# Kernel tuning notes

Measured on AMD Instinct MI355X. Metric: run time of the kernel, lower is better.

The kernel has to match this reference:

```python
import jax, jax.numpy as jnp
import numpy as np

N_NODES = 100000
N_EDGES = 3200000
IN_DIM, HID_DIM, LAT_DIM = 128, 64, 64


def gcn_conv(x, edge_index, W, b):
    """PyG-style GCNConv: add self-loops, symmetric deg^-1/2 normalization,
    linear transform, scatter-add aggregation, bias."""
    N = x.shape[0]
    loops = jnp.arange(N, dtype=edge_index.dtype)
    src = jnp.concatenate([edge_index[0], loops])  # [E+N]
    dst = jnp.concatenate([edge_index[1], loops])  # [E+N]
    # degree on target index (with self loops)
    deg = jax.ops.segment_sum(jnp.ones_like(dst, dtype=x.dtype), dst, num_segments=N)
    dinv = jnp.where(deg > 0, jax.lax.rsqrt(deg), 0.0)
    norm = dinv[src] * dinv[dst]  # [E+N]
    h = x @ W  # [N, out_dim] -- transform BEFORE gather (out_dim <= in_dim)
    msg = h[src] * norm[:, None]  # [E+N, out_dim]
    out = jax.ops.segment_sum(msg, dst, num_segments=N)
    return out + b


def setup_inputs() -> dict:
    key = jax.random.key(0)
    ks = jax.random.split(key, 6)
    x = jax.random.normal(ks[0], (N_NODES, IN_DIM), dtype=jnp.float32)
    edge_index = jax.random.randint(ks[1], (2, N_EDGES), 0, N_NODES, dtype=jnp.int64)
    # Glorot-ish init for weights, zero bias (PyG default)
    W1 = jax.random.normal(ks[2], (IN_DIM, HID_DIM), dtype=jnp.float32) / np.sqrt(IN_DIM)
    b1 = jnp.zeros((HID_DIM,), dtype=jnp.float32)
    W2 = jax.random.normal(ks[3], (HID_DIM, LAT_DIM), dtype=jnp.float32) / np.sqrt(HID_DIM)
    b2 = jnp.zeros((LAT_DIM,), dtype=jnp.float32)
    return {"x": x, "edge_index": edge_index, "W1": W1, "b1": b1, "W2": W2, "b2": b2}


def reference(x, edge_index, W1, b1, W2, b2):
    h = jax.nn.relu(gcn_conv(x, edge_index, W1, b1))
    return gcn_conv(h, edge_index, W2, b2)
```

## Files before the change

### kernel.cpp

```cpp
#include <hip/hip_runtime.h>
#include <cstdint>


#define BSHIFT 7
#define NBMAX 784
#define CH 8192
#define MAXB 6016

typedef __attribute__((ext_vector_type(8))) short bf16x8;
typedef __attribute__((ext_vector_type(4))) float f32x4;

__device__ inline unsigned short f2bf(float f) {
    unsigned u = __float_as_uint(f);
    unsigned r = (u + 0x7FFFu + ((u >> 16) & 1u)) >> 16;
    return (unsigned short)r;
}
__device__ inline unsigned pack2(float a, float b) {
    return (unsigned)f2bf(a) | ((unsigned)f2bf(b) << 16);
}
__device__ inline float blo(unsigned u) { return __uint_as_float(u << 16); }
__device__ inline float bhi(unsigned u) { return __uint_as_float(u & 0xFFFF0000u); }

__global__ __launch_bounds__(256) void hist_kernel(const int* __restrict__ dst,
                                                   int* __restrict__ histmat,
                                                   int E, int nb, int nblk,
                                                   const float* __restrict__ W1,
                                                   const float* __restrict__ W2,
                                                   unsigned short* __restrict__ W1t,
                                                   unsigned short* __restrict__ W2t) {
    if (blockIdx.x >= (unsigned)nblk) {
        int i = (blockIdx.x - nblk) * 256 + threadIdx.x;
        if (i < 128 * 64) {
            int k = i >> 6, n = i & 63;
            W1t[n * 128 + k] = f2bf(W1[i]);
        }
        int j = i - 128 * 64;
        if (j >= 0 && j < 64 * 64) {
            int k = j >> 6, n = j & 63;
            W2t[n * 64 + k] = f2bf(W2[j]);
        }
        return;
    }
    __shared__ int hist[NBMAX];
    int t = threadIdx.x;
    for (int b = t; b < nb; b += 256) hist[b] = 0;
    __syncthreads();
    int base = blockIdx.x * CH;
#pragma unroll
    for (int j = 0; j < CH / 1024; ++j) {
        int idx = base + j * 1024 + t * 4;
        if (idx + 4 <= E) {
            int4 d = *(const int4*)(dst + idx);
            atomicAdd(&hist[d.x >> BSHIFT], 1);
            atomicAdd(&hist[d.y >> BSHIFT], 1);
            atomicAdd(&hist[d.z >> BSHIFT], 1);
            atomicAdd(&hist[d.w >> BSHIFT], 1);
        } else {
            for (int k = 0; k < 4; ++k)
                if (idx + k < E) atomicAdd(&hist[dst[idx + k] >> BSHIFT], 1);
        }
    }
    __syncthreads();
    for (int b = t; b < nb; b += 256) histmat[blockIdx.x * nb + b] = hist[b];
}

__global__ __launch_bounds__(256) void scancol_kernel(const int* __restrict__ histmat,
                                                      int* __restrict__ colbase,
                                                      int* __restrict__ buckettotal,
                                                      int nb, int nblk) {
    __shared__ int ts[256];
    int b = blockIdx.x;
    int t = threadIdx.x;
    int v[4];
    int tsum = 0;
#pragma unroll
    for (int k = 0; k < 4; ++k) {
        int blk = t * 4 + k;
        v[k] = (blk < nblk) ? histmat[blk * nb + b] : 0;
        tsum += v[k];
    }
    ts[t] = tsum;
    __syncthreads();
    for (int ofs = 1; ofs < 256; ofs <<= 1) {
        int val = (t >= ofs) ? ts[t - ofs] : 0;
        __syncthreads();
        ts[t] += val;
        __syncthreads();
    }
    int run = ts[t] - tsum;
#pragma unroll
    for (int k = 0; k < 4; ++k) {
        int blk = t * 4 + k;
        if (blk < nblk) colbase[blk * nb + b] = run;
        run += v[k];
    }
    if (t == 255) buckettotal[b] = ts[255];
}

__global__ __launch_bounds__(256) void bscatter_kernel(const int* __restrict__ src,
                                                       const int* __restrict__ dst,
                                                       const int* __restrict__ colbase,
                                                       const int* __restrict__ buckettotal,
                                                       int* __restrict__ packed,
                                                       int E, int nb) {
    __shared__ int cur[NBMAX];
    __shared__ int ts2[256];
    int t = threadIdx.x;
    int v4[4];
    int tsum = 0;
#pragma unroll
    for (int k = 0; k < 4; ++k) {
        int bb = t * 4 + k;
        v4[k] = (bb < nb) ? buckettotal[bb] : 0;
        tsum += v4[k];
    }
    ts2[t] = tsum;
    __syncthreads();
    for (int ofs = 1; ofs < 256; ofs <<= 1) {
        int val = (t >= ofs) ? ts2[t - ofs] : 0;
        __syncthreads();
        ts2[t] += val;
        __syncthreads();
    }
    int run = ts2[t] - tsum;
#pragma unroll
    for (int k = 0; k < 4; ++k) {
        int bb = t * 4 + k;
        if (bb < nb) cur[bb] = run + colbase[blockIdx.x * nb + bb];
        run += v4[k];
    }
    __syncthreads();
    int base = blockIdx.x * CH;
#pragma unroll
    for (int j = 0; j < CH / 1024; ++j) {
        int idx = base + j * 1024 + t * 4;
        if (idx + 4 <= E) {
            int4 d = *(const int4*)(dst + idx);
            int4 s = *(const int4*)(src + idx);
            int p;
            p = atomicAdd(&cur[d.x >> BSHIFT], 1); packed[p] = ((d.x & 127) << 17) | s.x;
            p = atomicAdd(&cur[d.y >> BSHIFT], 1); packed[p] = ((d.y & 127) << 17) | s.y;
            p = atomicAdd(&cur[d.z >> BSHIFT], 1); packed[p] = ((d.z & 127) << 17) | s.z;
            p = atomicAdd(&cur[d.w >> BSHIFT], 1); packed[p] = ((d.w & 127) << 17) | s.w;
        } else {
            for (int k = 0; k < 4; ++k)
                if (idx + k < E) {
                    int dd = dst[idx + k], ss = src[idx + k];
                    int p = atomicAdd(&cur[dd >> BSHIFT], 1);
                    packed[p] = ((dd & 127) << 17) | ss;
                }
        }
    }
}

__global__ __launch_bounds__(256) void bcsr_kernel(const int* __restrict__ packed,
                                                   const int* __restrict__ buckettotal,
                                                   int* __restrict__ rowptr,
                                                   float* __restrict__ dinv,
                                                   int* __restrict__ csr,
                                                   int N, int nb) {
    __shared__ int deg[128];
    __shared__ int lrp[128];
    __shared__ int ts[128];
    __shared__ int ts2[256];
    __shared__ int shbb[2];
    __shared__ int ebuf[MAXB];
    __shared__ int obuf[MAXB];
    int b = blockIdx.x;
    int t = threadIdx.x;
    if (t < 128) deg[t] = 0;
    int v4[4];
    int tsum = 0;
#pragma unroll
    for (int k = 0; k < 4; ++k) {
        int bb = t * 4 + k;
        v4[k] = (bb < nb) ? buckettotal[bb] : 0;
        tsum += v4[k];
    }
    ts2[t] = tsum;
    __syncthreads();
    for (int ofs = 1; ofs < 256; ofs <<= 1) {
        int val = (t >= ofs) ? ts2[t - ofs] : 0;
        __syncthreads();
        ts2[t] += val;
        __syncthreads();
    }
    int run = ts2[t] - tsum;
#pragma unroll
    for (int k = 0; k < 4; ++k) {
        int bb = t * 4 + k;
        if (bb == b) { shbb[0] = run; shbb[1] = run + v4[k]; }
        run += v4[k];
    }
    __syncthreads();
    int bb0 = shbb[0];
    int bb1 = shbb[1];
    int cnt = bb1 - bb0;
    bool fits = (cnt <= MAXB);
    if (fits) {
        for (int i = t; i < cnt; i += 256) {
            int v = packed[bb0 + i];
            ebuf[i] = v;
            atomicAdd(&deg[v >> 17], 1);
        }
    } else {
        for (int i = t; i < cnt; i += 256)
            atomicAdd(&deg[packed[bb0 + i] >> 17], 1);
    }
    __syncthreads();
    if (t < 128) ts[t] = deg[t];
    __syncthreads();
    for (int ofs = 1; ofs < 128; ofs <<= 1) {
        int v = (t < 128 && t >= ofs) ? ts[t - ofs] : 0;
        __syncthreads();
        if (t < 128) ts[t] += v;
        __syncthreads();
    }
    int node0 = b << BSHIFT;
    int nlocal = min(128, N - node0);
    if (t < 128) lrp[t] = ts[t] - deg[t];
    if (t < nlocal) {
        rowptr[node0 + t] = bb0 + (ts[t] - deg[t]);
        dinv[node0 + t] = rsqrtf((float)(deg[t] + 1));
    }
    if (t == nlocal) rowptr[node0 + nlocal] = bb1;
    __syncthreads();
    if (fits) {
        for (int i = t; i < cnt; i += 256) {
            int v = ebuf[i];
            int p = atomicAdd(&lrp[v >> 17], 1);
            obuf[p] = v & 0x1FFFF;
        }
        __syncthreads();
        for (int i = t; i < cnt; i += 256) csr[bb0 + i] = obuf[i];
    } else {
        for (int i = t; i < cnt; i += 256) {
            int v = packed[bb0 + i];
            int p = atomicAdd(&lrp[v >> 17], 1);
            csr[bb0 + p] = v & 0x1FFFF;
        }
    }
}

template <int K, bool XBF16>
__global__ __launch_bounds__(256) void gemm_mfma(const void* __restrict__ Xv,
                                                 const unsigned short* __restrict__ Wt,
                                                 const float* __restrict__ dinv,
                                                 unsigned short* __restrict__ Ybf, int M) {
    constexpr int KP = K + 8;
    __shared__ unsigned short Xs[64 * KP];
    __shared__ unsigned short Ws[64 * KP];
    int t = threadIdx.x;
    int row0 = blockIdx.x * 64;

    for (int i = t; i < 64 * K / 8; i += 256) {
        int r = i / (K / 8), c8 = i % (K / 8);
        *(uint4*)(&Ws[r * KP + c8 * 8]) = ((const uint4*)Wt)[i];
    }
    if (XBF16) {
        const unsigned short* X = (const unsigned short*)Xv;
        for (int i = t; i < 64 * K / 8; i += 256) {
            int r = i / (K / 8), c8 = i % (K / 8);
            int gr = row0 + r;
            uint4 v = make_uint4(0u, 0u, 0u, 0u);
            if (gr < M) v = ((const uint4*)(X + (size_t)gr * K))[c8];
            *(uint4*)(&Xs[r * KP + c8 * 8]) = v;
        }
    } else {
        const float* X = (const float*)Xv;
        for (int i = t; i < 64 * K / 4; i += 256) {
            int r = i / (K / 4), c4 = i % (K / 4);
            int gr = row0 + r;
            float4 v = make_float4(0.f, 0.f, 0.f, 0.f);
            if (gr < M) v = ((const float4*)(X + (size_t)gr * K))[c4];
            uint2 p;
            p.x = pack2(v.x, v.y);
            p.y = pack2(v.z, v.w);
            *(uint2*)(&Xs[r * KP + c4 * 4]) = p;
        }
    }
    __syncthreads();

    int lane = t & 63;
    int w = t >> 6;
    int m = lane & 15;
    int q = lane >> 4;

    f32x4 acc[4];
#pragma unroll
    for (int nt = 0; nt < 4; ++nt) acc[nt] = (f32x4){0.f, 0.f, 0.f, 0.f};

#pragma unroll
    for (int s = 0; s < K / 32; ++s) {
        bf16x8 a = *(const bf16x8*)(&Xs[(16 * w + m) * KP + s * 32 + q * 8]);
#pragma unroll
        for (int nt = 0; nt < 4; ++nt) {
            bf16x8 b = *(const bf16x8*)(&Ws[(16 * nt + m) * KP + s * 32 + q * 8]);
            acc[nt] = __builtin_amdgcn_mfma_f32_16x16x32_bf16(a, b, acc[nt], 0, 0, 0);
        }
    }
    __syncthreads();

    unsigned short* Cs = Xs;
#pragma unroll
    for (int nt = 0; nt < 4; ++nt)
#pragma unroll
        for (int r = 0; r < 4; ++r) {
            int row = 16 * w + q * 4 + r;
            int gr = row0 + row;
            float d = (gr < M) ? dinv[gr] : 0.f;
            Cs[row * 72 + nt * 16 + m] = f2bf(acc[nt][r] * d);
        }
    __syncthreads();
    for (int i = t; i < 64 * 64 / 8; i += 256) {
        int r = i >> 3, c8 = i & 7;
        int gr = row0 + r;
        if (gr < M)
            *(uint4*)(Ybf + (size_t)gr * 64 + c8 * 8) = *(const uint4*)(&Cs[r * 72 + c8 * 8]);
    }
}

#define ACC8(v)                                      \
    acc[0] += blo(v.x); acc[1] += bhi(v.x);          \
    acc[2] += blo(v.y); acc[3] += bhi(v.y);          \
    acc[4] += blo(v.z); acc[5] += bhi(v.z);          \
    acc[6] += blo(v.w); acc[7] += bhi(v.w);

template <bool DO_GEMM>
__global__ __launch_bounds__(256) void aggregate_kernel(const unsigned* __restrict__ hsu,
                                                        const int* __restrict__ rowptr,
                                                        const int* __restrict__ csr,
                                                        const float* __restrict__ dinv,
                                                        const float* __restrict__ bias,
                                                        const unsigned short* __restrict__ W2t,
                                                        void* __restrict__ outv, int N) {
    __shared__ unsigned short Hs[DO_GEMM ? 32 * 72 : 1];
    __shared__ unsigned short W2s[DO_GEMM ? 64 * 72 : 1];
    __shared__ unsigned short Cs[DO_GEMM ? 32 * 72 : 1];
    int t = threadIdx.x;
    int node0 = blockIdx.x * 32;
    int node = node0 + (t >> 3);
    int sub = t & 7;
    int gbase = t & 56;

    if (DO_GEMM) {
        for (int i = t; i < 64 * 64 / 8; i += 256) {
            int r = i >> 3, c8 = i & 7;
            *(uint4*)(&W2s[r * 72 + c8 * 8]) = ((const uint4*)W2t)[i];
        }
    }

    float acc[8] = {0.f, 0.f, 0.f, 0.f, 0.f, 0.f, 0.f, 0.f};
    if (node < N) {
        {
            uint4 v = *(const uint4*)(hsu + (size_t)node * 32 + sub * 4);
            acc[0] = blo(v.x); acc[1] = bhi(v.x);
            acc[2] = blo(v.y); acc[3] = bhi(v.y);
            acc[4] = blo(v.z); acc[5] = bhi(v.z);
            acc[6] = blo(v.w); acc[7] = bhi(v.w);
        }
        int e0 = rowptr[node];
        int e1 = rowptr[node + 1];
        int e = e0;
        for (; e + 8 <= e1; e += 8) {
            int idx = csr[e + sub];
            int s0 = __shfl(idx, gbase + 0, 64);
            int s1 = __shfl(idx, gbase + 1, 64);
            int s2 = __shfl(idx, gbase + 2, 64);
            int s3 = __shfl(idx, gbase + 3, 64);
            int s4 = __shfl(idx, gbase + 4, 64);
            int s5 = __shfl(idx, gbase + 5, 64);
            int s6 = __shfl(idx, gbase + 6, 64);
            int s7 = __shfl(idx, gbase + 7, 64);
            uint4 v0 = *(const uint4*)(hsu + (size_t)s0 * 32 + sub * 4);
            uint4 v1 = *(const uint4*)(hsu + (size_t)s1 * 32 + sub * 4);
            uint4 v2 = *(const uint4*)(hsu + (size_t)s2 * 32 + sub * 4);
            uint4 v3 = *(const uint4*)(hsu + (size_t)s3 * 32 + sub * 4);
            uint4 v4 = *(const uint4*)(hsu + (size_t)s4 * 32 + sub * 4);
            uint4 v5 = *(const uint4*)(hsu + (size_t)s5 * 32 + sub * 4);
            uint4 v6 = *(const uint4*)(hsu + (size_t)s6 * 32 + sub * 4);
            uint4 v7 = *(const uint4*)(hsu + (size_t)s7 * 32 + sub * 4);
            ACC8(v0); ACC8(v1); ACC8(v2); ACC8(v3);
            ACC8(v4); ACC8(v5); ACC8(v6); ACC8(v7);
        }
        for (; e < e1; ++e) {
            int s = csr[e];
            uint4 v = *(const uint4*)(hsu + (size_t)s * 32 + sub * 4);
            ACC8(v);
        }
    }

    if (DO_GEMM) {
        if (node < N) {
            float d = dinv[node];
            float4 b0 = *(const float4*)(bias + sub * 8);
            float4 b1 = *(const float4*)(bias + sub * 8 + 4);
            float o[8];
            o[0] = fmaxf(fmaf(acc[0], d, b0.x), 0.f);
            o[1] = fmaxf(fmaf(acc[1], d, b0.y), 0.f);
            o[2] = fmaxf(fmaf(acc[2], d, b0.z), 0.f);
            o[3] = fmaxf(fmaf(acc[3], d, b0.w), 0.f);
            o[4] = fmaxf(fmaf(acc[4], d, b1.x), 0.f);
            o[5] = fmaxf(fmaf(acc[5], d, b1.y), 0.f);
            o[6] = fmaxf(fmaf(acc[6], d, b1.z), 0.f);
            o[7] = fmaxf(fmaf(acc[7], d, b1.w), 0.f);
            uint4 p;
            p.x = pack2(o[0], o[1]); p.y = pack2(o[2], o[3]);
            p.z = pack2(o[4], o[5]); p.w = pack2(o[6], o[7]);
            *(uint4*)(&Hs[(t >> 3) * 72 + sub * 8]) = p;
        }
        __syncthreads();
        int lane = t & 63;
        int w = t >> 6;
        int m = lane & 15;
        int q = lane >> 4;
        int mt = w & 1;
#pragma unroll
        for (int half = 0; half < 2; ++half) {
            int nt = (w >> 1) + half * 2;
            f32x4 a4 = (f32x4){0.f, 0.f, 0.f, 0.f};
#pragma unroll
            for (int s = 0; s < 2; ++s) {
                bf16x8 a = *(const bf16x8*)(&Hs[(mt * 16 + m) * 72 + s * 32 + q * 8]);
                bf16x8 b = *(const bf16x8*)(&W2s[(nt * 16 + m) * 72 + s * 32 + q * 8]);
                a4 = __builtin_amdgcn_mfma_f32_16x16x32_bf16(a, b, a4, 0, 0, 0);
            }
#pragma unroll
            for (int r = 0; r < 4; ++r) {
                int row = mt * 16 + q * 4 + r;
                int gn = node0 + row;
                float dd = (gn < N) ? dinv[gn] : 0.f;
                Cs[row * 72 + nt * 16 + m] = f2bf(a4[r] * dd);
            }
        }
        __syncthreads();
        unsigned short* outb = (unsigned short*)outv;
        for (int i = t; i < 32 * 64 / 8; i += 256) {
            int r = i >> 3, c8 = i & 7;
            int gn = node0 + r;
            if (gn < N)
                *(uint4*)(outb + (size_t)gn * 64 + c8 * 8) = *(const uint4*)(&Cs[r * 72 + c8 * 8]);
        }
    } else {
        if (node >= N) return;
        float d = dinv[node];
        float4 b0 = *(const float4*)(bias + sub * 8);
        float4 b1 = *(const float4*)(bias + sub * 8 + 4);
        float o[8];
        o[0] = fmaf(acc[0], d, b0.x); o[1] = fmaf(acc[1], d, b0.y);
        o[2] = fmaf(acc[2], d, b0.z); o[3] = fmaf(acc[3], d, b0.w);
        o[4] = fmaf(acc[4], d, b1.x); o[5] = fmaf(acc[5], d, b1.y);
        o[6] = fmaf(acc[6], d, b1.z); o[7] = fmaf(acc[7], d, b1.w);
        float* op = (float*)outv + (size_t)node * 64 + sub * 8;
        *(float4*)(op)     = make_float4(o[0], o[1], o[2], o[3]);
        *(float4*)(op + 4) = make_float4(o[4], o[5], o[6], o[7]);
    }
}

extern "C" void kernel_launch(void* const* d_in, const int* in_sizes, int n_in,
                              void* d_out, int out_size, void* d_ws, size_t ws_size,
                              hipStream_t stream) {
    const float* x  = (const float*)d_in[0];
    const int*   ei = (const int*)d_in[1];
    const float* W1 = (const float*)d_in[2];
    const float* b1 = (const float*)d_in[3];
    const float* W2 = (const float*)d_in[4];
    const float* b2 = (const float*)d_in[5];

    const int N = in_sizes[0] / 128;
    const int E = in_sizes[1] / 2;
    const int* src = ei;
    const int* dst = ei + E;
    float* out = (float*)d_out;

    const int nb   = (N + 127) >> BSHIFT;
    const int nblk = (E + CH - 1) / CH;

    char* ws = (char*)d_ws;
    size_t off = 0;
    auto alloc = [&](size_t bytes) -> char* {
        char* p = ws + off;
        off = (off + bytes + 255) & ~(size_t)255;
        return p;
    };
    int*   csr         = (int*)alloc((size_t)E * 4);
    int*   rowptr      = (int*)alloc((size_t)(N + 1) * 4);
    float* dinv        = (float*)alloc((size_t)N * 4);
    int*   buckettotal = (int*)alloc((size_t)nb * 4);
    unsigned short* W1t = (unsigned short*)alloc(64 * 128 * 2);
    unsigned short* W2t = (unsigned short*)alloc(64 * 64 * 2);
    unsigned short* bufA = (unsigned short*)alloc((size_t)N * 64 * 2);
    unsigned short* bufB = (unsigned short*)alloc((size_t)N * 64 * 2);
    int* histmat = (int*)bufA;
    int* packed  = (int*)((char*)bufA + ((size_t)nblk * nb * 4 + 255 & ~(size_t)255) + 256);

    hist_kernel<<<nblk + 48, 256, 0, stream>>>(dst, histmat, E, nb, nblk, W1, W2, W1t, W2t);
    scancol_kernel<<<nb, 256, 0, stream>>>(histmat, histmat, buckettotal, nb, nblk);
    bscatter_kernel<<<nblk, 256, 0, stream>>>(src, dst, histmat, buckettotal, packed, E, nb);
    bcsr_kernel<<<nb, 256, 0, stream>>>(packed, buckettotal, rowptr, dinv, csr, N, nb);

    gemm_mfma<128, false><<<(N + 63) / 64, 256, 0, stream>>>(x, W1t, dinv, bufA, N);
    aggregate_kernel<true><<<(N + 31) / 32, 256, 0, stream>>>((const unsigned*)bufA, rowptr,
                                                              csr, dinv, b1, W2t, bufB, N);
    aggregate_kernel<false><<<(N + 31) / 32, 256, 0, stream>>>((const unsigned*)bufB, rowptr,
                                                               csr, dinv, b2, W2t, out, N);
}
```

Baseline: 310.2 us.

## Compute degrees in histogram pass and fuse bucket scatter with first GEMM

Per-node degrees are now counted with global atomics during the histogram pass, so dinv can be written early in the column-scan kernel. That lets the first GEMM run in the same launch as the bucket scatter. The scatter blocks now handle larger chunks of edges, and bcsr no longer counts degrees itself. The layer-1 aggregate now does its W2 matmul per wave, with register shuffles instead of a block-wide shared tile. The cost is 3.2M extra global atomics, an extra memset, and reuse of the csr and bufB buffers as scratch.

```diff
diff --git a/kernel.cpp b/kernel.cpp
--- a/kernel.cpp
+++ b/kernel.cpp
@@ -4,11 +4,14 @@
 
 #define BSHIFT 7
 #define NBMAX 784
-#define CH 8192
+#define CHH 8192
+#define CHC 32768
 #define MAXB 6016
 
 typedef __attribute__((ext_vector_type(8))) short bf16x8;
 typedef __attribute__((ext_vector_type(4))) float f32x4;
+
+union U8 { unsigned u[4]; bf16x8 v; };
 
 __device__ inline unsigned short f2bf(float f) {
     unsigned u = __float_as_uint(f);
@@ -27,7 +30,8 @@
                                                    const float* __restrict__ W1,
                                                    const float* __restrict__ W2,
                                                    unsigned short* __restrict__ W1t,
-                                                   unsigned short* __restrict__ W2t) {
+                                                   unsigned short* __restrict__ W2t,
+                                                   int* __restrict__ deg_g) {
     if (blockIdx.x >= (unsigned)nblk) {
         int i = (blockIdx.x - nblk) * 256 + threadIdx.x;
         if (i < 128 * 64) {
@@ -45,9 +49,9 @@
     int t = threadIdx.x;
     for (int b = t; b < nb; b += 256) hist[b] = 0;
     __syncthreads();
-    int base = blockIdx.x * CH;
-#pragma unroll
-    for (int j = 0; j < CH / 1024; ++j) {
+    int base = blockIdx.x * CHH;
+#pragma unroll
+    for (int j = 0; j < CHH / 1024; ++j) {
         int idx = base + j * 1024 + t * 4;
         if (idx + 4 <= E) {
             int4 d = *(const int4*)(dst + idx);
@@ -55,9 +59,17 @@
             atomicAdd(&hist[d.y >> BSHIFT], 1);
             atomicAdd(&hist[d.z >> BSHIFT], 1);
             atomicAdd(&hist[d.w >> BSHIFT], 1);
+            atomicAdd(&deg_g[d.x], 1);
+            atomicAdd(&deg_g[d.y], 1);
+            atomicAdd(&deg_g[d.z], 1);
+            atomicAdd(&deg_g[d.w], 1);
         } else {
             for (int k = 0; k < 4; ++k)
-                if (idx + k < E) atomicAdd(&hist[dst[idx + k] >> BSHIFT], 1);
+                if (idx + k < E) {
+                    int dd = dst[idx + k];
+                    atomicAdd(&hist[dd >> BSHIFT], 1);
+                    atomicAdd(&deg_g[dd], 1);
+                }
         }
     }
     __syncthreads();
@@ -67,10 +79,16 @@
 __global__ __launch_bounds__(256) void scancol_kernel(const int* __restrict__ histmat,
                                                       int* __restrict__ colbase,
                                                       int* __restrict__ buckettotal,
-                                                      int nb, int nblk) {
+                                                      int nb, int nblk,
+                                                      const int* __restrict__ deg_g,
+                                                      float* __restrict__ dinv, int N) {
     __shared__ int ts[256];
     int b = blockIdx.x;
     int t = threadIdx.x;
+    if (t < 128) {
+        int node = b * 128 + t;
+        if (node < N) dinv[node] = rsqrtf((float)(deg_g[node] + 1));
+    }
     int v[4];
     int tsum = 0;
 #pragma unroll
@@ -97,15 +115,86 @@
     if (t == 255) buckettotal[b] = ts[255];
 }
 
-__global__ __launch_bounds__(256) void bscatter_kernel(const int* __restrict__ src,
-                                                       const int* __restrict__ dst,
-                                                       const int* __restrict__ colbase,
-                                                       const int* __restrict__ buckettotal,
-                                                       int* __restrict__ packed,
-                                                       int E, int nb) {
-    __shared__ int cur[NBMAX];
-    __shared__ int ts2[256];
-    int t = threadIdx.x;
+__device__ void gemm1_body(char* smem, const float* __restrict__ X,
+                           const unsigned short* __restrict__ Wt,
+                           const float* __restrict__ dinv,
+                           unsigned short* __restrict__ Ybf, int M, int blk) {
+    constexpr int K = 128, KP = 136;
+    unsigned short* Xs = (unsigned short*)smem;
+    unsigned short* Ws = Xs + 64 * KP;
+    int t = threadIdx.x;
+    int row0 = blk * 64;
+
+    for (int i = t; i < 64 * K / 8; i += 256) {
+        int r = i / (K / 8), c8 = i % (K / 8);
+        *(uint4*)(&Ws[r * KP + c8 * 8]) = ((const uint4*)Wt)[i];
+    }
+    for (int i = t; i < 64 * K / 4; i += 256) {
+        int r = i / (K / 4), c4 = i % (K / 4);
+        int gr = row0 + r;
+        float4 v = make_float4(0.f, 0.f, 0.f, 0.f);
+        if (gr < M) v = ((const float4*)(X + (size_t)gr * K))[c4];
+        uint2 p;
+        p.x = pack2(v.x, v.y);
+        p.y = pack2(v.z, v.w);
+        *(uint2*)(&Xs[r * KP + c4 * 4]) = p;
+    }
+    __syncthreads();
+
+    int lane = t & 63;
+    int w = t >> 6;
+    int m = lane & 15;
+    int q = lane >> 4;
+
+    f32x4 acc[4];
+#pragma unroll
+    for (int nt = 0; nt < 4; ++nt) acc[nt] = (f32x4){0.f, 0.f, 0.f, 0.f};
+
+#pragma unroll
+    for (int s = 0; s < K / 32; ++s) {
+        bf16x8 a = *(const bf16x8*)(&Xs[(16 * w + m) * KP + s * 32 + q * 8]);
+#pragma unroll
+        for (int nt = 0; nt < 4; ++nt) {
+            bf16x8 b = *(const bf16x8*)(&Ws[(16 * nt + m) * KP + s * 32 + q * 8]);
+            acc[nt] = __builtin_amdgcn_mfma_f32_16x16x32_bf16(a, b, acc[nt], 0, 0, 0);
+        }
+    }
+    __syncthreads();
+
+    unsigned short* Cs = Xs;
+#pragma unroll
+    for (int nt = 0; nt < 4; ++nt)
+#pragma unroll
+        for (int r = 0; r < 4; ++r) {
+            int row = 16 * w + q * 4 + r;
+            int gr = row0 + row;
+            float d = (gr < M) ? dinv[gr] : 0.f;
+            Cs[row * 72 + nt * 16 + m] = f2bf(acc[nt][r] * d);
+        }
+    __syncthreads();
+    for (int i = t; i < 64 * 64 / 8; i += 256) {
+        int r = i >> 3, c8 = i & 7;
+        int gr = row0 + r;
+        if (gr < M)
+            *(uint4*)(Ybf + (size_t)gr * 64 + c8 * 8) = *(const uint4*)(&Cs[r * 72 + c8 * 8]);
+    }
+}
+
+__global__ __launch_bounds__(256) void bscatter_gemm1_kernel(
+        const int* __restrict__ src, const int* __restrict__ dst,
+        const int* __restrict__ colbase, const int* __restrict__ buckettotal,
+        int* __restrict__ packed, int E, int nb, int nblkc,
+        const float* __restrict__ x, const unsigned short* __restrict__ W1t,
+        const float* __restrict__ dinv, unsigned short* __restrict__ bufA, int N) {
+    __shared__ char smem[2 * 64 * 136 * 2];
+    int t = threadIdx.x;
+    if ((int)blockIdx.x >= nblkc) {
+        gemm1_body(smem, x, W1t, dinv, bufA, N, (int)blockIdx.x - nblkc);
+        return;
+    }
+    int* cur = (int*)smem;
+    int* ts2 = cur + NBMAX;
+    int c0 = (int)blockIdx.x * (CHC / CHH);
     int v4[4];
     int tsum = 0;
 #pragma unroll
@@ -126,13 +215,13 @@
 #pragma unroll
     for (int k = 0; k < 4; ++k) {
         int bb = t * 4 + k;
-        if (bb < nb) cur[bb] = run + colbase[blockIdx.x * nb + bb];
+        if (bb < nb) cur[bb] = run + colbase[(size_t)c0 * nb + bb];
         run += v4[k];
     }
     __syncthreads();
-    int base = blockIdx.x * CH;
-#pragma unroll
-    for (int j = 0; j < CH / 1024; ++j) {
+    int base = (int)blockIdx.x * CHC;
+#pragma unroll 4
+    for (int j = 0; j < CHC / 1024; ++j) {
         int idx = base + j * 1024 + t * 4;
         if (idx + 4 <= E) {
             int4 d = *(const int4*)(dst + idx);
@@ -142,7 +231,7 @@
             p = atomicAdd(&cur[d.y >> BSHIFT], 1); packed[p] = ((d.y & 127) << 17) | s.y;
             p = atomicAdd(&cur[d.z >> BSHIFT], 1); packed[p] = ((d.z & 127) << 17) | s.z;
             p = atomicAdd(&cur[d.w >> BSHIFT], 1); packed[p] = ((d.w & 127) << 17) | s.w;
-        } else {
+        } else if (idx < E) {
             for (int k = 0; k < 4; ++k)
                 if (idx + k < E) {
                     int dd = dst[idx + k], ss = src[idx + k];
@@ -155,8 +244,8 @@
 
 __global__ __launch_bounds__(256) void bcsr_kernel(const int* __restrict__ packed,
                                                    const int* __restrict__ buckettotal,
+                                                   const int* __restrict__ deg_g,
                                                    int* __restrict__ rowptr,
-                                                   float* __restrict__ dinv,
                                                    int* __restrict__ csr,
                                                    int N, int nb) {
     __shared__ int deg[128];
@@ -168,7 +257,11 @@
     __shared__ int obuf[MAXB];
     int b = blockIdx.x;
     int t = threadIdx.x;
-    if (t < 128) deg[t] = 0;
+    int node0 = b << BSHIFT;
+    if (t < 128) {
+        int node = node0 + t;
+        deg[t] = (node < N) ? deg_g[node] : 0;
+    }
     int v4[4];
     int tsum = 0;
 #pragma unroll
@@ -198,16 +291,8 @@
     int cnt = bb1 - bb0;
     bool fits = (cnt <= MAXB);
     if (fits) {
-        for (int i = t; i < cnt; i += 256) {
-            int v = packed[bb0 + i];
-            ebuf[i] = v;
-            atomicAdd(&deg[v >> 17], 1);
-        }
-    } else {
-        for (int i = t; i < cnt; i += 256)
-            atomicAdd(&deg[packed[bb0 + i] >> 17], 1);
-    }
-    __syncthreads();
+        for (int i = t; i < cnt; i += 256) ebuf[i] = packed[bb0 + i];
+    }
     if (t < 128) ts[t] = deg[t];
     __syncthreads();
     for (int ofs = 1; ofs < 128; ofs <<= 1) {
@@ -216,13 +301,9 @@
         if (t < 128) ts[t] += v;
         __syncthreads();
     }
-    int node0 = b << BSHIFT;
     int nlocal = min(128, N - node0);
     if (t < 128) lrp[t] = ts[t] - deg[t];
-    if (t < nlocal) {
-        rowptr[node0 + t] = bb0 + (ts[t] - deg[t]);
-        dinv[node0 + t] = rsqrtf((float)(deg[t] + 1));
-    }
+    if (t < nlocal) rowptr[node0 + t] = bb0 + (ts[t] - deg[t]);
     if (t == nlocal) rowptr[node0 + nlocal] = bb1;
     __syncthreads();
     if (fits) {
@@ -242,219 +323,160 @@
     }
 }
 
-template <int K, bool XBF16>
-__global__ __launch_bounds__(256) void gemm_mfma(const void* __restrict__ Xv,
-                                                 const unsigned short* __restrict__ Wt,
-                                                 const float* __restrict__ dinv,
-                                                 unsigned short* __restrict__ Ybf, int M) {
-    constexpr int KP = K + 8;
-    __shared__ unsigned short Xs[64 * KP];
-    __shared__ unsigned short Ws[64 * KP];
-    int t = threadIdx.x;
-    int row0 = blockIdx.x * 64;
-
-    for (int i = t; i < 64 * K / 8; i += 256) {
-        int r = i / (K / 8), c8 = i % (K / 8);
-        *(uint4*)(&Ws[r * KP + c8 * 8]) = ((const uint4*)Wt)[i];
-    }
-    if (XBF16) {
-        const unsigned short* X = (const unsigned short*)Xv;
-        for (int i = t; i < 64 * K / 8; i += 256) {
-            int r = i / (K / 8), c8 = i % (K / 8);
-            int gr = row0 + r;
-            uint4 v = make_uint4(0u, 0u, 0u, 0u);
-            if (gr < M) v = ((const uint4*)(X + (size_t)gr * K))[c8];
-            *(uint4*)(&Xs[r * KP + c8 * 8]) = v;
-        }
-    } else {
-        const float* X = (const float*)Xv;
-        for (int i = t; i < 64 * K / 4; i += 256) {
-            int r = i / (K / 4), c4 = i % (K / 4);
-            int gr = row0 + r;
-            float4 v = make_float4(0.f, 0.f, 0.f, 0.f);
-            if (gr < M) v = ((const float4*)(X + (size_t)gr * K))[c4];
-            uint2 p;
-            p.x = pack2(v.x, v.y);
-            p.y = pack2(v.z, v.w);
-            *(uint2*)(&Xs[r * KP + c4 * 4]) = p;
-        }
-    }
-    __syncthreads();
-
-    int lane = t & 63;
-    int w = t >> 6;
-    int m = lane & 15;
-    int q = lane >> 4;
-
-    f32x4 acc[4];
-#pragma unroll
-    for (int nt = 0; nt < 4; ++nt) acc[nt] = (f32x4){0.f, 0.f, 0.f, 0.f};
-
-#pragma unroll
-    for (int s = 0; s < K / 32; ++s) {
-        bf16x8 a = *(const bf16x8*)(&Xs[(16 * w + m) * KP + s * 32 + q * 8]);
-#pragma unroll
-        for (int nt = 0; nt < 4; ++nt) {
-            bf16x8 b = *(const bf16x8*)(&Ws[(16 * nt + m) * KP + s * 32 + q * 8]);
-            acc[nt] = __builtin_amdgcn_mfma_f32_16x16x32_bf16(a, b, acc[nt], 0, 0, 0);
-        }
-    }
-    __syncthreads();
-
-    unsigned short* Cs = Xs;
-#pragma unroll
-    for (int nt = 0; nt < 4; ++nt)
-#pragma unroll
-        for (int r = 0; r < 4; ++r) {
-            int row = 16 * w + q * 4 + r;
-            int gr = row0 + row;
-            float d = (gr < M) ? dinv[gr] : 0.f;
-            Cs[row * 72 + nt * 16 + m] = f2bf(acc[nt][r] * d);
-        }
-    __syncthreads();
-    for (int i = t; i < 64 * 64 / 8; i += 256) {
-        int r = i >> 3, c8 = i & 7;
-        int gr = row0 + r;
-        if (gr < M)
-            *(uint4*)(Ybf + (size_t)gr * 64 + c8 * 8) = *(const uint4*)(&Cs[r * 72 + c8 * 8]);
-    }
-}
-
 #define ACC8(v)                                      \
     acc[0] += blo(v.x); acc[1] += bhi(v.x);          \
     acc[2] += blo(v.y); acc[3] += bhi(v.y);          \
     acc[4] += blo(v.z); acc[5] += bhi(v.z);          \
     acc[6] += blo(v.w); acc[7] += bhi(v.w);
 
-template <bool DO_GEMM>
-__global__ __launch_bounds__(256) void aggregate_kernel(const unsigned* __restrict__ hsu,
-                                                        const int* __restrict__ rowptr,
-                                                        const int* __restrict__ csr,
-                                                        const float* __restrict__ dinv,
-                                                        const float* __restrict__ bias,
-                                                        const unsigned short* __restrict__ W2t,
-                                                        void* __restrict__ outv, int N) {
-    __shared__ unsigned short Hs[DO_GEMM ? 32 * 72 : 1];
-    __shared__ unsigned short W2s[DO_GEMM ? 64 * 72 : 1];
-    __shared__ unsigned short Cs[DO_GEMM ? 32 * 72 : 1];
-    int t = threadIdx.x;
+#define GATHER_BODY                                                     \
+    {                                                                   \
+        uint4 v = *(const uint4*)(hsu + (size_t)node * 32 + sub * 4);   \
+        acc[0] = blo(v.x); acc[1] = bhi(v.x);                           \
+        acc[2] = blo(v.y); acc[3] = bhi(v.y);                           \
+        acc[4] = blo(v.z); acc[5] = bhi(v.z);                           \
+        acc[6] = blo(v.w); acc[7] = bhi(v.w);                           \
+    }                                                                   \
+    int e0 = rowptr[node];                                              \
+    int e1 = rowptr[node + 1];                                          \
+    int e = e0;                                                         \
+    for (; e + 8 <= e1; e += 8) {                                       \
+        int idx = csr[e + sub];                                         \
+        int s0 = __shfl(idx, gbase + 0, 64);                            \
+        int s1 = __shfl(idx, gbase + 1, 64);                            \
+        int s2 = __shfl(idx, gbase + 2, 64);                            \
+        int s3 = __shfl(idx, gbase + 3, 64);                            \
+        int s4 = __shfl(idx, gbase + 4, 64);                            \
+        int s5 = __shfl(idx, gbase + 5, 64);                            \
+        int s6 = __shfl(idx, gbase + 6, 64);                            \
+        int s7 = __shfl(idx, gbase + 7, 64);                            \
+        uint4 v0 = *(const uint4*)(hsu + (size_t)s0 * 32 + sub * 4);    \
+        uint4 v1 = *(const uint4*)(hsu + (size_t)s1 * 32 + sub * 4);    \
+        uint4 v2 = *(const uint4*)(hsu + (size_t)s2 * 32 + sub * 4);    \
+        uint4 v3 = *(const uint4*)(hsu + (size_t)s3 * 32 + sub * 4);    \
+        uint4 v4 = *(const uint4*)(hsu + (size_t)s4 * 32 + sub * 4);    \
+        uint4 v5 = *(const uint4*)(hsu + (size_t)s5 * 32 + sub * 4);    \
+        uint4 v6 = *(const uint4*)(hsu + (size_t)s6 * 32 + sub * 4);    \
+        uint4 v7 = *(const uint4*)(hsu + (size_t)s7 * 32 + sub * 4);    \
+        ACC8(v0); ACC8(v1); ACC8(v2); ACC8(v3);                         \
+        ACC8(v4); ACC8(v5); ACC8(v6); ACC8(v7);                         \
+    }                                                                   \
+    for (; e < e1; ++e) {                                               \
+        int s = csr[e];                                                 \
+        uint4 v = *(const uint4*)(hsu + (size_t)s * 32 + sub * 4);      \
+        ACC8(v);                                                        \
+    }
+
+__global__ __launch_bounds__(256) void aggregate_gemm_kernel(
+        const unsigned* __restrict__ hsu, const int* __restrict__ rowptr,
+        const int* __restrict__ csr, const float* __restrict__ dinv,
+        const float* __restrict__ bias, const unsigned short* __restrict__ W2t,
+        unsigned short* __restrict__ outb, int N) {
+    __shared__ unsigned short W2s[64 * 72];
+    __shared__ unsigned short Cs[4][8 * 72];
+    int t = threadIdx.x;
+    for (int i = t; i < 64 * 64 / 8; i += 256) {
+        int r = i >> 3, c8 = i & 7;
+        *(uint4*)(&W2s[r * 72 + c8 * 8]) = ((const uint4*)W2t)[i];
+    }
+    __syncthreads();
+
     int node0 = blockIdx.x * 32;
     int node = node0 + (t >> 3);
     int sub = t & 7;
     int gbase = t & 56;
 
-    if (DO_GEMM) {
-        for (int i = t; i < 64 * 64 / 8; i += 256) {
-            int r = i >> 3, c8 = i & 7;
-            *(uint4*)(&W2s[r * 72 + c8 * 8]) = ((const uint4*)W2t)[i];
-        }
-    }
-
     float acc[8] = {0.f, 0.f, 0.f, 0.f, 0.f, 0.f, 0.f, 0.f};
+    uint4 pk = make_uint4(0u, 0u, 0u, 0u);
     if (node < N) {
-        {
-            uint4 v = *(const uint4*)(hsu + (size_t)node * 32 + sub * 4);
-            acc[0] = blo(v.x); acc[1] = bhi(v.x);
-            acc[2] = blo(v.y); acc[3] = bhi(v.y);
-            acc[4] = blo(v.z); acc[5] = bhi(v.z);
-            acc[6] = blo(v.w); acc[7] = bhi(v.w);
-        }
-        int e0 = rowptr[node];
-        int e1 = rowptr[node + 1];
-        int e = e0;
-        for (; e + 8 <= e1; e += 8) {
-            int idx = csr[e + sub];
-            int s0 = __shfl(idx, gbase + 0, 64);
-            int s1 = __shfl(idx, gbase + 1, 64);
-            int s2 = __shfl(idx, gbase + 2, 64);
-            int s3 = __shfl(idx, gbase + 3, 64);
-            int s4 = __shfl(idx, gbase + 4, 64);
-            int s5 = __shfl(idx, gbase + 5, 64);
-            int s6 = __shfl(idx, gbase + 6, 64);
-            int s7 = __shfl(idx, gbase + 7, 64);
-            uint4 v0 = *(const uint4*)(hsu + (size_t)s0 * 32 + sub * 4);
-            uint4 v1 = *(const uint4*)(hsu + (size_t)s1 * 32 + sub * 4);
-            uint4 v2 = *(const uint4*)(hsu + (size_t)s2 * 32 + sub * 4);
-            uint4 v3 = *(const uint4*)(hsu + (size_t)s3 * 32 + sub * 4);
-            uint4 v4 = *(const uint4*)(hsu + (size_t)s4 * 32 + sub * 4);
-            uint4 v5 = *(const uint4*)(hsu + (size_t)s5 * 32 + sub * 4);
-            uint4 v6 = *(const uint4*)(hsu + (size_t)s6 * 32 + sub * 4);
-            uint4 v7 = *(const uint4*)(hsu + (size_t)s7 * 32 + sub * 4);
-            ACC8(v0); ACC8(v1); ACC8(v2); ACC8(v3);
-            ACC8(v4); ACC8(v5); ACC8(v6); ACC8(v7);
-        }
-        for (; e < e1; ++e) {
-            int s = csr[e];
-            uint4 v = *(const uint4*)(hsu + (size_t)s * 32 + sub * 4);
-            ACC8(v);
-        }
-    }
-
-    if (DO_GEMM) {
-        if (node < N) {
-            float d = dinv[node];
-            float4 b0 = *(const float4*)(bias + sub * 8);
-            float4 b1 = *(const float4*)(bias + sub * 8 + 4);
-            float o[8];
-            o[0] = fmaxf(fmaf(acc[0], d, b0.x), 0.f);
-            o[1] = fmaxf(fmaf(acc[1], d, b0.y), 0.f);
-            o[2] = fmaxf(fmaf(acc[2], d, b0.z), 0.f);
-            o[3] = fmaxf(fmaf(acc[3], d, b0.w), 0.f);
-            o[4] = fmaxf(fmaf(acc[4], d, b1.x), 0.f);
-            o[5] = fmaxf(fmaf(acc[5], d, b1.y), 0.f);
-            o[6] = fmaxf(fmaf(acc[6], d, b1.z), 0.f);
-            o[7] = fmaxf(fmaf(acc[7], d, b1.w), 0.f);
-            uint4 p;
-            p.x = pack2(o[0], o[1]); p.y = pack2(o[2], o[3]);
-            p.z = pack2(o[4], o[5]); p.w = pack2(o[6], o[7]);
-            *(uint4*)(&Hs[(t >> 3) * 72 + sub * 8]) = p;
-        }
-        __syncthreads();
-        int lane = t & 63;
-        int w = t >> 6;
-        int m = lane & 15;
-        int q = lane >> 4;
-        int mt = w & 1;
-#pragma unroll
-        for (int half = 0; half < 2; ++half) {
-            int nt = (w >> 1) + half * 2;
-            f32x4 a4 = (f32x4){0.f, 0.f, 0.f, 0.f};
-#pragma unroll
-            for (int s = 0; s < 2; ++s) {
-                bf16x8 a = *(const bf16x8*)(&Hs[(mt * 16 + m) * 72 + s * 32 + q * 8]);
-                bf16x8 b = *(const bf16x8*)(&W2s[(nt * 16 + m) * 72 + s * 32 + q * 8]);
-                a4 = __builtin_amdgcn_mfma_f32_16x16x32_bf16(a, b, a4, 0, 0, 0);
-            }
-#pragma unroll
-            for (int r = 0; r < 4; ++r) {
-                int row = mt * 16 + q * 4 + r;
-                int gn = node0 + row;
-                float dd = (gn < N) ? dinv[gn] : 0.f;
-                Cs[row * 72 + nt * 16 + m] = f2bf(a4[r] * dd);
-            }
-        }
-        __syncthreads();
-        unsigned short* outb = (unsigned short*)outv;
-        for (int i = t; i < 32 * 64 / 8; i += 256) {
-            int r = i >> 3, c8 = i & 7;
-            int gn = node0 + r;
-            if (gn < N)
-                *(uint4*)(outb + (size_t)gn * 64 + c8 * 8) = *(const uint4*)(&Cs[r * 72 + c8 * 8]);
-        }
-    } else {
-        if (node >= N) return;
+        GATHER_BODY
         float d = dinv[node];
         float4 b0 = *(const float4*)(bias + sub * 8);
         float4 b1 = *(const float4*)(bias + sub * 8 + 4);
-        float o[8];
-        o[0] = fmaf(acc[0], d, b0.x); o[1] = fmaf(acc[1], d, b0.y);
-        o[2] = fmaf(acc[2], d, b0.z); o[3] = fmaf(acc[3], d, b0.w);
-        o[4] = fmaf(acc[4], d, b1.x); o[5] = fmaf(acc[5], d, b1.y);
-        o[6] = fmaf(acc[6], d, b1.z); o[7] = fmaf(acc[7], d, b1.w);
-        float* op = (float*)outv + (size_t)node * 64 + sub * 8;
-        *(float4*)(op)     = make_float4(o[0], o[1], o[2], o[3]);
-        *(float4*)(op + 4) = make_float4(o[4], o[5], o[6], o[7]);
-    }
+        float o0 = fmaxf(fmaf(acc[0], d, b0.x), 0.f);
+        float o1 = fmaxf(fmaf(acc[1], d, b0.y), 0.f);
+        float o2 = fmaxf(fmaf(acc[2], d, b0.z), 0.f);
+        float o3 = fmaxf(fmaf(acc[3], d, b0.w), 0.f);
+        float o4 = fmaxf(fmaf(acc[4], d, b1.x), 0.f);
+        float o5 = fmaxf(fmaf(acc[5], d, b1.y), 0.f);
+        float o6 = fmaxf(fmaf(acc[6], d, b1.z), 0.f);
+        float o7 = fmaxf(fmaf(acc[7], d, b1.w), 0.f);
+        pk.x = pack2(o0, o1); pk.y = pack2(o2, o3);
+        pk.z = pack2(o4, o5); pk.w = pack2(o6, o7);
+    }
+
+    int lane = t & 63;
+    int m16 = lane & 15;
+    int q = lane >> 4;
+    int wv = t >> 6;
+    int wnode0 = node0 + wv * 8;
+    bool am = (m16 < 8);
+    int sl0 = ((m16 & 7) << 3) + q;
+    int sl1 = sl0 + 4;
+    unsigned a00 = (unsigned)__shfl((int)pk.x, sl0, 64);
+    unsigned a01 = (unsigned)__shfl((int)pk.y, sl0, 64);
+    unsigned a02 = (unsigned)__shfl((int)pk.z, sl0, 64);
+    unsigned a03 = (unsigned)__shfl((int)pk.w, sl0, 64);
+    unsigned a10 = (unsigned)__shfl((int)pk.x, sl1, 64);
+    unsigned a11 = (unsigned)__shfl((int)pk.y, sl1, 64);
+    unsigned a12 = (unsigned)__shfl((int)pk.z, sl1, 64);
+    unsigned a13 = (unsigned)__shfl((int)pk.w, sl1, 64);
+    U8 fa0, fa1;
+    fa0.u[0] = am ? a00 : 0u;
+    fa0.u[1] = am ? a01 : 0u;
+    fa0.u[2] = am ? a02 : 0u;
+    fa0.u[3] = am ? a03 : 0u;
+    fa1.u[0] = am ? a10 : 0u;
+    fa1.u[1] = am ? a11 : 0u;
+    fa1.u[2] = am ? a12 : 0u;
+    fa1.u[3] = am ? a13 : 0u;
+
+    unsigned short* Cw = &Cs[wv][0];
+#pragma unroll
+    for (int nt = 0; nt < 4; ++nt) {
+        bf16x8 bb0 = *(const bf16x8*)(&W2s[(nt * 16 + m16) * 72 + q * 8]);
+        bf16x8 bb1 = *(const bf16x8*)(&W2s[(nt * 16 + m16) * 72 + 32 + q * 8]);
+        f32x4 c4 = (f32x4){0.f, 0.f, 0.f, 0.f};
+        c4 = __builtin_amdgcn_mfma_f32_16x16x32_bf16(fa0.v, bb0, c4, 0, 0, 0);
+        c4 = __builtin_amdgcn_mfma_f32_16x16x32_bf16(fa1.v, bb1, c4, 0, 0, 0);
+        if (q < 2) {
+#pragma unroll
+            for (int r = 0; r < 4; ++r) {
+                int row = q * 4 + r;
+                int gn = wnode0 + row;
+                float dd = (gn < N) ? dinv[gn] : 0.f;
+                Cw[row * 72 + nt * 16 + m16] = f2bf(c4[r] * dd);
+            }
+        }
+    }
+    int row = lane >> 3, c8 = lane & 7;
+    int gn = wnode0 + row;
+    if (gn < N)
+        *(uint4*)(outb + (size_t)gn * 64 + c8 * 8) = *(const uint4*)(&Cw[row * 72 + c8 * 8]);
+}
+
+__global__ __launch_bounds__(256) void aggregate_out_kernel(
+        const unsigned* __restrict__ hsu, const int* __restrict__ rowptr,
+        const int* __restrict__ csr, const float* __restrict__ dinv,
+        const float* __restrict__ bias, float* __restrict__ outv, int N) {
+    int t = threadIdx.x;
+    int node = blockIdx.x * 32 + (t >> 3);
+    if (node >= N) return;
+    int sub = t & 7;
+    int gbase = t & 56;
+    float acc[8];
+    GATHER_BODY
+    float d = dinv[node];
+    float4 b0 = *(const float4*)(bias + sub * 8);
+    float4 b1 = *(const float4*)(bias + sub * 8 + 4);
+    float o[8];
+    o[0] = fmaf(acc[0], d, b0.x); o[1] = fmaf(acc[1], d, b0.y);
+    o[2] = fmaf(acc[2], d, b0.z); o[3] = fmaf(acc[3], d, b0.w);
+    o[4] = fmaf(acc[4], d, b1.x); o[5] = fmaf(acc[5], d, b1.y);
+    o[6] = fmaf(acc[6], d, b1.z); o[7] = fmaf(acc[7], d, b1.w);
+    float* op = outv + (size_t)node * 64 + sub * 8;
+    *(float4*)(op)     = make_float4(o[0], o[1], o[2], o[3]);
+    *(float4*)(op + 4) = make_float4(o[4], o[5], o[6], o[7]);
 }
 
 extern "C" void kernel_launch(void* const* d_in, const int* in_sizes, int n_in,
@@ -473,8 +495,10 @@
     const int* dst = ei + E;
     float* out = (float*)d_out;
 
-    const int nb   = (N + 127) >> BSHIFT;
-    const int nblk = (E + CH - 1) / CH;
+    const int nb    = (N + 127) >> BSHIFT;
+    const int nblkh = (E + CHH - 1) / CHH;
+    const int nblkc = (E + CHC - 1) / CHC;
+    const int ngemm1 = (N + 63) / 64;
 
     char* ws = (char*)d_ws;
     size_t off = 0;
@@ -486,22 +510,26 @@
     int*   csr         = (int*)alloc((size_t)E * 4);
     int*   rowptr      = (int*)alloc((size_t)(N + 1) * 4);
     float* dinv        = (float*)alloc((size_t)N * 4);
+    int*   deg_g       = (int*)alloc((size_t)N * 4);
     int*   buckettotal = (int*)alloc((size_t)nb * 4);
     unsigned short* W1t = (unsigned short*)alloc(64 * 128 * 2);
     unsigned short* W2t = (unsigned short*)alloc(64 * 64 * 2);
     unsigned short* bufA = (unsigned short*)alloc((size_t)N * 64 * 2);
     unsigned short* bufB = (unsigned short*)alloc((size_t)N * 64 * 2);
-    int* histmat = (int*)bufA;
-    int* packed  = (int*)((char*)bufA + ((size_t)nblk * nb * 4 + 255 & ~(size_t)255) + 256);
-
-    hist_kernel<<<nblk + 48, 256, 0, stream>>>(dst, histmat, E, nb, nblk, W1, W2, W1t, W2t);
-    scancol_kernel<<<nb, 256, 0, stream>>>(histmat, histmat, buckettotal, nb, nblk);
-    bscatter_kernel<<<nblk, 256, 0, stream>>>(src, dst, histmat, buckettotal, packed, E, nb);
-    bcsr_kernel<<<nb, 256, 0, stream>>>(packed, buckettotal, rowptr, dinv, csr, N, nb);
-
-    gemm_mfma<128, false><<<(N + 63) / 64, 256, 0, stream>>>(x, W1t, dinv, bufA, N);
-    aggregate_kernel<true><<<(N + 31) / 32, 256, 0, stream>>>((const unsigned*)bufA, rowptr,
-                                                              csr, dinv, b1, W2t, bufB, N);
-    aggregate_kernel<false><<<(N + 31) / 32, 256, 0, stream>>>((const unsigned*)bufB, rowptr,
-                                                               csr, dinv, b2, W2t, out, N);
-}
+    int* histmat = csr;
+    int* packed  = (int*)bufB;
+
+    hipMemsetAsync(deg_g, 0, (size_t)N * 4, stream);
+    hist_kernel<<<nblkh + 48, 256, 0, stream>>>(dst, histmat, E, nb, nblkh,
+                                                W1, W2, W1t, W2t, deg_g);
+    scancol_kernel<<<nb, 256, 0, stream>>>(histmat, histmat, buckettotal, nb, nblkh,
+                                           deg_g, dinv, N);
+    bscatter_gemm1_kernel<<<nblkc + ngemm1, 256, 0, stream>>>(
+        src, dst, histmat, buckettotal, packed, E, nb, nblkc, x, W1t, dinv, bufA, N);
+    bcsr_kernel<<<nb, 256, 0, stream>>>(packed, buckettotal, deg_g, rowptr, csr, N, nb);
+
+    aggregate_gemm_kernel<<<(N + 31) / 32, 256, 0, stream>>>(
+        (const unsigned*)bufA, rowptr, csr, dinv, b1, W2t, bufB, N);
+    aggregate_out_kernel<<<(N + 31) / 32, 256, 0, stream>>>(
+        (const unsigned*)bufB, rowptr, csr, dinv, b2, out, N);
+}
```

After: 444.5 us. +43.3%, slower.
